# Optimization experiments

Measured on AMD Instinct MI355X. Metric: run time of the kernel, lower is better.

Reference implementation:

```python
import jax, jax.numpy as jnp
import numpy as np

D_MODEL = 2048
D_HEAD = 64
Q_HEADS = 32
KV_HEADS = 8


def rope(x):
    # x: [B, S, H, D], rotate interleaved pairs along last dim
    B, S, H, D = x.shape
    pos = jnp.arange(S, dtype=x.dtype)
    freq = 1.0 / (10000.0 ** (jnp.arange(0, D, 2, dtype=x.dtype) / D))  # [D/2]
    theta = pos[:, None] * freq[None, :]                                 # [S, D/2]
    cos = jnp.cos(theta)[None, :, None, :]
    sin = jnp.sin(theta)[None, :, None, :]
    xr = x.reshape(B, S, H, D // 2, 2)
    x1, x2 = xr[..., 0], xr[..., 1]
    out = jnp.stack((x1 * cos - x2 * sin, x1 * sin + x2 * cos), axis=-1)
    return out.reshape(B, S, H, D)


def setup_inputs() -> dict:
    key = jax.random.key(0)
    ks = jax.random.split(key, 7)
    x = jax.random.normal(ks[0], (1, 2048, D_MODEL), dtype=jnp.float32)
    W_q = jax.random.normal(ks[1], (Q_HEADS * D_HEAD, D_MODEL), dtype=jnp.float32) * 0.02
    b_q = jnp.zeros((Q_HEADS * D_HEAD,), dtype=jnp.float32)
    W_kv = jax.random.normal(ks[2], (2 * KV_HEADS * D_HEAD, D_MODEL), dtype=jnp.float32) * 0.02
    b_kv = jnp.zeros((2 * KV_HEADS * D_HEAD,), dtype=jnp.float32)
    W_out = jax.random.normal(ks[3], (D_MODEL, D_MODEL), dtype=jnp.float32) * 0.02
    b_out = jnp.zeros((D_MODEL,), dtype=jnp.float32)
    return {"x": x, "W_q": W_q, "b_q": b_q, "W_kv": W_kv, "b_kv": b_kv,
            "W_out": W_out, "b_out": b_out}


def reference(x, W_q, b_q, W_kv, b_kv, W_out, b_out):
    B, S, _ = x.shape
    g = Q_HEADS // KV_HEADS
    Q = (x @ W_q.T + b_q).reshape(B, S, Q_HEADS, D_HEAD)
    kv = x @ W_kv.T + b_kv
    K, V = jnp.split(kv, 2, axis=-1)
    K = K.reshape(B, S, KV_HEADS, D_HEAD)
    V = V.reshape(B, S, KV_HEADS, D_HEAD)
    Q = rope(Q)
    K = rope(K)
    K = jnp.repeat(K, g, axis=2)  # [B, S, Q_HEADS, D_HEAD]
    V = jnp.repeat(V, g, axis=2)
    scale = 1.0 / (D_HEAD ** 0.5)
    scores = jnp.einsum('bqhd,bkhd->bhqk', Q, K) * scale  # [B,H,S,S]
    # note: original calls non-inplace masked_fill and discards it, so no causal mask applied
    probs = jax.nn.softmax(scores, axis=-1)
    attn = jnp.einsum('bhqk,bkhd->bqhd', probs, V).reshape(B, S, D_MODEL)
    return attn @ W_out.T + b_out
```

## Files before the change

### kernel.cpp

```cpp
#include <hip/hip_runtime.h>
#include <hip/hip_bf16.h>
#include <math.h>

#define S_LEN 2048
#define D_MODEL 2048
#define Q_HEADS 32
#define KV_HEADS 8

typedef __attribute__((ext_vector_type(8))) short short8;
typedef __attribute__((ext_vector_type(4))) float f32x4;

__device__ __forceinline__ short bf16_rne(float f) {
  unsigned u = __float_as_uint(f);
  unsigned r = (u + 0x7FFFu + ((u >> 16) & 1u)) >> 16;
  return (short)r;
}
__device__ __forceinline__ void dma16(const short* g, short* l) {
  __builtin_amdgcn_global_load_lds(
      (const __attribute__((address_space(1))) void*)g,
      (__attribute__((address_space(3))) void*)l, 16, 0, 0);
}
__device__ __forceinline__ void fast_sincos(float theta, float& sn, float& cs) {
  double rev = (double)theta * 0.15915494309189535;
  float fr = (float)(rev - floor(rev));
  sn = __builtin_amdgcn_sinf(fr);
  cs = __builtin_amdgcn_cosf(fr);
}
__device__ __forceinline__ void cvt8(const float* src, short* dst, int i) {
  float4 a = *(const float4*)&src[i];
  float4 b = *(const float4*)&src[i + 4];
  short8 h;
  h[0] = bf16_rne(a.x); h[1] = bf16_rne(a.y);
  h[2] = bf16_rne(a.z); h[3] = bf16_rne(a.w);
  h[4] = bf16_rne(b.x); h[5] = bf16_rne(b.y);
  h[6] = bf16_rne(b.z); h[7] = bf16_rne(b.w);
  *(short8*)&dst[i] = h;
}

#define NM (2048 * 2048)
#define NKV (1024 * 2048)

__global__ __launch_bounds__(256) void cvt_all(
    const float* __restrict__ x,    short* __restrict__ xh,
    const float* __restrict__ wq,   short* __restrict__ wqh,
    const float* __restrict__ wkv,  short* __restrict__ wkvh,
    const float* __restrict__ wo,   short* __restrict__ woh,
    float* __restrict__ freqTab) {
  if (blockIdx.x == 0 && threadIdx.x < 32) {
    const double e = (2.0 * threadIdx.x) / 64.0;
    freqTab[threadIdx.x] = (float)pow(10000.0, -e);
  }
  int i = (blockIdx.x * 256 + threadIdx.x) * 8;
  if (i < NM) { cvt8(x, xh, i); return; }
  i -= NM;
  if (i < NM) { cvt8(wq, wqh, i); return; }
  i -= NM;
  if (i < NKV) { cvt8(wkv, wkvh, i); return; }
  i -= NKV;
  cvt8(wo, woh, i);
}

#define QSCALE 0.18033688011112042f

__global__ __launch_bounds__(256) void gemm_qkv_rope(
    const short* __restrict__ Ah,
    const short* __restrict__ Bq, const short* __restrict__ Bkv,
    const float* __restrict__ bq, const float* __restrict__ bkv,
    const float* __restrict__ tab,
    short* __restrict__ Qrm, short* __restrict__ Krm,
    short* __restrict__ Vt) {
  const int Nq = 2048, K = 2048;
  __shared__ short As[2][128 * 32];
  __shared__ short Bs[2][64 * 32];
  const int tid = threadIdx.x;
  const int w = tid >> 6, lane = tid & 63;
  const int l16 = lane & 15, quad = lane >> 4;

  const int b = blockIdx.x;
  const int r = b & 7, ri = b >> 3;
  const int bx = (r & 3) * 12 + ri % 12;
  const int by = (r >> 2) * 8 + ri / 12;
  const int bm = by * 128;
  const int bnG = bx * 64;

  const short* Bsrc; const float* bias; int bn;
  if (bnG < Nq) { Bsrc = Bq;  bias = bq;  bn = bnG; }
  else          { Bsrc = Bkv; bias = bkv; bn = bnG - Nq; }
  const int mode = (bnG < Nq) ? 0 : ((bnG < Nq + 512) ? 1 : 2);

  const int drow0 = w * 16 + (lane >> 2);
  const int drow1 = drow0 + 64;
  const int slot = lane & 3;
  const int ch0 = slot ^ ((drow0 >> 1) & 3);
  const int ch1 = slot ^ ((drow1 >> 1) & 3);
  const size_t a0 = (size_t)(bm + drow0) * K + ch0 * 8;
  const size_t a1 = (size_t)(bm + drow1) * K + ch1 * 8;
  const size_t b0 = (size_t)(bn + drow0) * K + ch0 * 8;
  const int dA0 = (w * 16) * 32, dA1 = (64 + w * 16) * 32;

  const int wm = (w & 1) * 64, wn = (w >> 1) * 32;
  int offA[4], offB[2];
#pragma unroll
  for (int i = 0; i < 4; ++i) {
    int R = wm + i * 16 + l16;
    offA[i] = R * 32 + (quad ^ ((R >> 1) & 3)) * 8;
  }
#pragma unroll
  for (int j = 0; j < 2; ++j) {
    int R = wn + j * 16 + l16;
    offB[j] = R * 32 + (quad ^ ((R >> 1) & 3)) * 8;
  }

  f32x4 acc[4][2];
#pragma unroll
  for (int i = 0; i < 4; ++i)
#pragma unroll
    for (int j = 0; j < 2; ++j)
#pragma unroll
      for (int e = 0; e < 4; ++e) acc[i][j][e] = 0.f;

  const int T = K / 32;
  dma16(Ah + a0, &As[0][dA0]);
  dma16(Ah + a1, &As[0][dA1]);
  dma16(Bsrc + b0, &Bs[0][dA0]);
  __syncthreads();

  for (int t = 0; t < T; ++t) {
    const int cur = t & 1, nxt = cur ^ 1;
    if (t + 1 < T) {
      const int ko = (t + 1) * 32;
      dma16(Ah + a0 + ko, &As[nxt][dA0]);
      dma16(Ah + a1 + ko, &As[nxt][dA1]);
      dma16(Bsrc + b0 + ko, &Bs[nxt][dA0]);
    }
    short8 af[4], bf[2];
#pragma unroll
    for (int i = 0; i < 4; ++i) af[i] = *(const short8*)&As[cur][offA[i]];
#pragma unroll
    for (int j = 0; j < 2; ++j) bf[j] = *(const short8*)&Bs[cur][offB[j]];
#pragma unroll
    for (int i = 0; i < 4; ++i)
#pragma unroll
      for (int j = 0; j < 2; ++j)
        acc[i][j] = __builtin_amdgcn_mfma_f32_16x16x32_bf16(af[i], bf[j], acc[i][j], 0, 0, 0);
    __syncthreads();
  }

#pragma unroll
  for (int i = 0; i < 4; ++i) {
    const int row0 = bm + wm + i * 16 + quad * 4;
#pragma unroll
    for (int j = 0; j < 2; ++j) {
      const int col = bn + wn + j * 16 + l16;
      const float bv = bias[col];
      if (mode == 2) {
        const int d = col - 512;
        short4 sv;
        sv.x = bf16_rne(acc[i][j][0] + bv);
        sv.y = bf16_rne(acc[i][j][1] + bv);
        sv.z = bf16_rne(acc[i][j][2] + bv);
        sv.w = bf16_rne(acc[i][j][3] + bv);
        *(short4*)&Vt[(size_t)d * S_LEN + row0] = sv;
      } else {
        const float fr = tab[(col & 63) >> 1];
        const float sgn = (col & 1) ? 1.f : -1.f;
#pragma unroll
        for (int e = 0; e < 4; ++e) {
          float v = acc[i][j][e] + bv;
          float other = __shfl_xor(v, 1);
          float sn, cs;
          fast_sincos((float)(row0 + e) * fr, sn, cs);
          const float o = v * cs + sgn * other * sn;
          if (mode == 0)
            Qrm[(size_t)(row0 + e) * D_MODEL + col] = bf16_rne(o * QSCALE);
          else
            Krm[(size_t)(row0 + e) * 512 + col] = bf16_rne(o);
        }
      }
    }
  }
}

__global__ __launch_bounds__(256) void gemm_nt1_big(
    const short* __restrict__ A, const short* __restrict__ B,
    const float* __restrict__ bias, float* __restrict__ C,
    int N, int K) {
  __shared__ short As[2][128 * 32];
  __shared__ short Bs[2][128 * 32];
  const int tid = threadIdx.x;
  const int w = tid >> 6, lane = tid & 63;
  const int l16 = lane & 15, quad = lane >> 4;

  const int b = blockIdx.x;
  const int r = b & 7, ri = b >> 3;
  const int bx = (r & 1) * 8 + ri % 8;
  const int by = (r >> 1) * 4 + ri / 8;
  const int bm = by * 128;
  const int bn = bx * 128;

  const int drow0 = w * 16 + (lane >> 2);
  const int drow1 = drow0 + 64;
  const int slot = lane & 3;
  const int ch0 = slot ^ ((drow0 >> 1) & 3);
  const int ch1 = slot ^ ((drow1 >> 1) & 3);
  const short* gA0 = &A[(size_t)(bm + drow0) * K + ch0 * 8];
  const short* gA1 = &A[(size_t)(bm + drow1) * K + ch1 * 8];
  const short* gB0 = &B[(size_t)(bn + drow0) * K + ch0 * 8];
  const short* gB1 = &B[(size_t)(bn + drow1) * K + ch1 * 8];
  const int dA0 = (w * 16) * 32, dA1 = (64 + w * 16) * 32;

  const int wm = (w & 1) * 64, wn = (w >> 1) * 64;
  int offA[4], offB[4];
#pragma unroll
  for (int i = 0; i < 4; ++i) {
    int R = wm + i * 16 + l16;
    offA[i] = R * 32 + (quad ^ ((R >> 1) & 3)) * 8;
    int Rb = wn + i * 16 + l16;
    offB[i] = Rb * 32 + (quad ^ ((Rb >> 1) & 3)) * 8;
  }

  f32x4 acc[4][4];
#pragma unroll
  for (int i = 0; i < 4; ++i)
#pragma unroll
    for (int j = 0; j < 4; ++j)
#pragma unroll
      for (int e = 0; e < 4; ++e) acc[i][j][e] = 0.f;

  const int T = K / 32;
  dma16(gA0, &As[0][dA0]);
  dma16(gA1, &As[0][dA1]);
  dma16(gB0, &Bs[0][dA0]);
  dma16(gB1, &Bs[0][dA1]);
  __syncthreads();

  for (int t = 0; t < T; ++t) {
    const int cur = t & 1, nxt = cur ^ 1;
    if (t + 1 < T) {
      const int ko = (t + 1) * 32;
      dma16(gA0 + ko, &As[nxt][dA0]);
      dma16(gA1 + ko, &As[nxt][dA1]);
      dma16(gB0 + ko, &Bs[nxt][dA0]);
      dma16(gB1 + ko, &Bs[nxt][dA1]);
    }
    short8 af[4], bf[4];
#pragma unroll
    for (int i = 0; i < 4; ++i) af[i] = *(const short8*)&As[cur][offA[i]];
#pragma unroll
    for (int j = 0; j < 4; ++j) bf[j] = *(const short8*)&Bs[cur][offB[j]];
#pragma unroll
    for (int i = 0; i < 4; ++i)
#pragma unroll
      for (int j = 0; j < 4; ++j)
        acc[i][j] = __builtin_amdgcn_mfma_f32_16x16x32_bf16(af[i], bf[j], acc[i][j], 0, 0, 0);
    __syncthreads();
  }

#pragma unroll
  for (int i = 0; i < 4; ++i) {
#pragma unroll
    for (int j = 0; j < 4; ++j) {
      const int col = bn + wn + j * 16 + l16;
      const float bv = bias[col];
      const int row0 = bm + wm + i * 16 + quad * 4;
#pragma unroll
      for (int e = 0; e < 4; ++e)
        C[(size_t)(row0 + e) * N + col] = acc[i][j][e] + bv;
    }
  }
}

__global__ __launch_bounds__(256, 4) void flash8(
    const short* __restrict__ Qrm, const short* __restrict__ Krm,
    const short* __restrict__ Vt, short* __restrict__ Oh) {
  const int qt = blockIdx.x, h = blockIdx.y;
  const int kvh = h >> 2;
  const int tid = threadIdx.x;
  const int w = tid >> 6, lane = tid & 63;
  const int l16 = lane & 15, quad = lane >> 4;

  __shared__ short Ks[2][64 * 64];
  __shared__ short Vs[2][64 * 64];
  __shared__ short Ps[64 * 64];

  const short* Vh = Vt + (size_t)kvh * 64 * S_LEN;
  const int qr = qt * 64 + w * 16 + l16;

  short8 qf0 = *(const short8*)&Qrm[(size_t)qr * D_MODEL + h * 64 + quad * 8];
  short8 qf1 = *(const short8*)&Qrm[(size_t)qr * D_MODEL + h * 64 + 32 + quad * 8];

  short8 ones;
#pragma unroll
  for (int e = 0; e < 8; ++e) ones[e] = (short)0x3F80;

  const int drow = lane >> 3;
  const int ch = (lane & 7) ^ drow;
  const short* gK = &Krm[(size_t)(w * 16 + drow) * 512 + kvh * 64 + ch * 8];
  const short* gV = &Vh[(size_t)(w * 16 + drow) * S_LEN + ch * 8];

  const int sl0 = quad ^ (l16 & 7);
  int offT[4][2];
#pragma unroll
  for (int m = 0; m < 4; ++m) {
    offT[m][0] = (m * 16 + l16) * 64 + sl0 * 8;
    offT[m][1] = (m * 16 + l16) * 64 + (sl0 ^ 4) * 8;
  }

  const int prow = (w * 16 + l16) * 64;
  const int pswz = (l16 & 7) << 1;
  int pwr[4];
#pragma unroll
  for (int m = 0; m < 4; ++m) pwr[m] = prow + ((4 * m + quad) ^ pswz) * 4;
  const int prd0 = prow + ((2 * quad) ^ pswz) * 4;
  const int prd1 = prow + ((8 + 2 * quad) ^ pswz) * 4;

  f32x4 accl;
#pragma unroll
  for (int e = 0; e < 4; ++e) accl[e] = 0.f;
  f32x4 acco[4];
#pragma unroll
  for (int m = 0; m < 4; ++m)
#pragma unroll
    for (int e = 0; e < 4; ++e) acco[m][e] = 0.f;

  dma16(gK,               &Ks[0][(w * 16) * 64]);
  dma16(gK + 8 * 512,     &Ks[0][(w * 16 + 8) * 64]);
  dma16(gV,               &Vs[0][(w * 16) * 64]);
  dma16(gV + 8 * S_LEN,   &Vs[0][(w * 16 + 8) * 64]);
  __syncthreads();

  for (int t = 0; t < 32; ++t) {
    const int cur = t & 1, nxt = cur ^ 1;
    if (t + 1 < 32) {
      const short* gKn = gK + (size_t)(t + 1) * 64 * 512;
      const short* gVn = gV + (t + 1) * 64;
      dma16(gKn,             &Ks[nxt][(w * 16) * 64]);
      dma16(gKn + 8 * 512,   &Ks[nxt][(w * 16 + 8) * 64]);
      dma16(gVn,             &Vs[nxt][(w * 16) * 64]);
      dma16(gVn + 8 * S_LEN, &Vs[nxt][(w * 16 + 8) * 64]);
    }

    const short* kc = Ks[cur];
    f32x4 accs[4];
#pragma unroll
    for (int m = 0; m < 4; ++m)
#pragma unroll
      for (int e = 0; e < 4; ++e) accs[m][e] = 0.f;
#pragma unroll
    for (int m = 0; m < 4; ++m) {
      short8 k0 = *(const short8*)&kc[offT[m][0]];
      short8 k1 = *(const short8*)&kc[offT[m][1]];
      accs[m] = __builtin_amdgcn_mfma_f32_16x16x32_bf16(k0, qf0, accs[m], 0, 0, 0);
      accs[m] = __builtin_amdgcn_mfma_f32_16x16x32_bf16(k1, qf1, accs[m], 0, 0, 0);
    }

#pragma unroll
    for (int m = 0; m < 4; ++m) {
      float p0 = exp2f(accs[m][0]);
      float p1 = exp2f(accs[m][1]);
      float p2 = exp2f(accs[m][2]);
      float p3 = exp2f(accs[m][3]);
      unsigned u01 = __builtin_amdgcn_perm(__float_as_uint(p1), __float_as_uint(p0), 0x07060302u);
      unsigned u23 = __builtin_amdgcn_perm(__float_as_uint(p3), __float_as_uint(p2), 0x07060302u);
      *(uint2*)&Ps[pwr[m]] = make_uint2(u01, u23);
    }

    short8 pf0 = *(const short8*)&Ps[prd0];
    short8 pf1 = *(const short8*)&Ps[prd1];
    accl = __builtin_amdgcn_mfma_f32_16x16x32_bf16(ones, pf0, accl, 0, 0, 0);
    accl = __builtin_amdgcn_mfma_f32_16x16x32_bf16(ones, pf1, accl, 0, 0, 0);
    const short* vc = Vs[cur];
#pragma unroll
    for (int m = 0; m < 4; ++m) {
      short8 v0 = *(const short8*)&vc[offT[m][0]];
      short8 v1 = *(const short8*)&vc[offT[m][1]];
      acco[m] = __builtin_amdgcn_mfma_f32_16x16x32_bf16(v0, pf0, acco[m], 0, 0, 0);
      acco[m] = __builtin_amdgcn_mfma_f32_16x16x32_bf16(v1, pf1, acco[m], 0, 0, 0);
    }

    __syncthreads();
  }

  const float inv = 1.f / accl[0];
#pragma unroll
  for (int m = 0; m < 4; ++m) {
    short4 h4;
    h4.x = bf16_rne(acco[m][0] * inv);
    h4.y = bf16_rne(acco[m][1] * inv);
    h4.z = bf16_rne(acco[m][2] * inv);
    h4.w = bf16_rne(acco[m][3] * inv);
    const size_t base = (size_t)qr * D_MODEL + h * 64 + m * 16 + quad * 4;
    *(short4*)&Oh[base] = h4;
  }
}

extern "C" void kernel_launch(void* const* d_in, const int* in_sizes, int n_in,
                              void* d_out, int out_size, void* d_ws, size_t ws_size,
                              hipStream_t stream) {
  const float* x     = (const float*)d_in[0];
  const float* W_q   = (const float*)d_in[1];
  const float* b_q   = (const float*)d_in[2];
  const float* W_kv  = (const float*)d_in[3];
  const float* b_kv  = (const float*)d_in[4];
  const float* W_out = (const float*)d_in[5];
  const float* b_out = (const float*)d_in[6];
  float* out = (float*)d_out;

  char* ws = (char*)d_ws;
  short* xh    = (short*)(ws);
  short* Wqh   = (short*)(ws + (8u << 20));
  short* Wkvh  = (short*)(ws + (16u << 20));
  short* Woh   = (short*)(ws + (20u << 20));
  short* Qrm   = (short*)(ws + (28u << 20));
  short* Krm   = (short*)(ws + (36u << 20));
  short* Vtb   = (short*)(ws + (38u << 20));
  float* freqTab = (float*)(ws + (40u << 20));
  short* Ath   = xh;

  cvt_all<<<7168, 256, 0, stream>>>(x, xh, W_q, Wqh, W_kv, Wkvh, W_out, Woh,
                                    freqTab);

  gemm_qkv_rope<<<768, 256, 0, stream>>>(
      xh, Wqh, Wkvh, b_q, b_kv, freqTab, Qrm, Krm, Vtb);

  flash8<<<dim3(S_LEN / 64, Q_HEADS), 256, 0, stream>>>(Qrm, Krm, Vtb, Ath);

  gemm_nt1_big<<<256, 256, 0, stream>>>(Ath, Woh, b_out, out, 2048, 2048);
}
```

Measured before the change: 256.3 us.

## Double flash attention KV tile to 128 keys per iteration

The attention kernel now processes 128 keys per loop iteration instead of 64, halving the number of iterations and barriers. K, V and P shared buffers double in size, with new swizzled offsets and DMA addressing for the wider V tile. Score accumulation is fused per 16-key block so exp2 and P stores follow each MFMA pair directly. LDS use doubles and launch bounds drop to 2 blocks per CU, which may reduce occupancy and latency hiding.

```diff
diff --git a/kernel.cpp b/kernel.cpp
--- a/kernel.cpp
+++ b/kernel.cpp
@@ -270,7 +270,7 @@
   }
 }
 
-__global__ __launch_bounds__(256, 4) void flash8(
+__global__ __launch_bounds__(256, 2) void flash9(
     const short* __restrict__ Qrm, const short* __restrict__ Krm,
     const short* __restrict__ Vt, short* __restrict__ Oh) {
   const int qt = blockIdx.x, h = blockIdx.y;
@@ -279,9 +279,9 @@
   const int w = tid >> 6, lane = tid & 63;
   const int l16 = lane & 15, quad = lane >> 4;
 
-  __shared__ short Ks[2][64 * 64];
-  __shared__ short Vs[2][64 * 64];
-  __shared__ short Ps[64 * 64];
+  __shared__ short Ks[2][128 * 64];
+  __shared__ short Vs[2][64 * 128];
+  __shared__ short Ps[64 * 128];
 
   const short* Vh = Vt + (size_t)kvh * 64 * S_LEN;
   const int qr = qt * 64 + w * 16 + l16;
@@ -293,26 +293,42 @@
 #pragma unroll
   for (int e = 0; e < 8; ++e) ones[e] = (short)0x3F80;
 
-  const int drow = lane >> 3;
-  const int ch = (lane & 7) ^ drow;
-  const short* gK = &Krm[(size_t)(w * 16 + drow) * 512 + kvh * 64 + ch * 8];
-  const short* gV = &Vh[(size_t)(w * 16 + drow) * S_LEN + ch * 8];
+  f32x4 fz;
+#pragma unroll
+  for (int e = 0; e < 4; ++e) fz[e] = 0.f;
+
+  const int drK = lane >> 3;
+  const short* gK = &Krm[(size_t)(w * 32 + drK) * 512 + kvh * 64 +
+                         ((lane & 7) ^ drK) * 8];
+  const int drV = lane >> 4;
+  const short* gVa = &Vh[(size_t)(w * 16 + drV) * S_LEN +
+                         (((lane & 15) ^ drV)) * 8];
+  const short* gVb = &Vh[(size_t)(w * 16 + drV) * S_LEN +
+                         (((lane & 15) ^ drV ^ 4)) * 8];
 
   const int sl0 = quad ^ (l16 & 7);
-  int offT[4][2];
-#pragma unroll
-  for (int m = 0; m < 4; ++m) {
-    offT[m][0] = (m * 16 + l16) * 64 + sl0 * 8;
-    offT[m][1] = (m * 16 + l16) * 64 + (sl0 ^ 4) * 8;
-  }
-
-  const int prow = (w * 16 + l16) * 64;
+  int offK[8][2];
+#pragma unroll
+  for (int m = 0; m < 8; ++m) {
+    offK[m][0] = (m * 16 + l16) * 64 + sl0 * 8;
+    offK[m][1] = (m * 16 + l16) * 64 + (sl0 ^ 4) * 8;
+  }
+  int offV[4][4];
+#pragma unroll
+  for (int m = 0; m < 4; ++m)
+#pragma unroll
+    for (int ks = 0; ks < 4; ++ks)
+      offV[m][ks] = (m * 16 + l16) * 128 + ((4 * ks + quad) ^ (l16 & 7)) * 8;
+
+  const int prow = (w * 16 + l16) * 128;
   const int pswz = (l16 & 7) << 1;
-  int pwr[4];
-#pragma unroll
-  for (int m = 0; m < 4; ++m) pwr[m] = prow + ((4 * m + quad) ^ pswz) * 4;
-  const int prd0 = prow + ((2 * quad) ^ pswz) * 4;
-  const int prd1 = prow + ((8 + 2 * quad) ^ pswz) * 4;
+  int pwr[8];
+#pragma unroll
+  for (int m = 0; m < 8; ++m) pwr[m] = prow + ((4 * m + quad) ^ pswz) * 4;
+  int prd[4];
+#pragma unroll
+  for (int ks = 0; ks < 4; ++ks)
+    prd[ks] = prow + ((8 * ks + 2 * quad) ^ pswz) * 4;
 
   f32x4 accl;
 #pragma unroll
@@ -323,59 +339,61 @@
 #pragma unroll
     for (int e = 0; e < 4; ++e) acco[m][e] = 0.f;
 
-  dma16(gK,               &Ks[0][(w * 16) * 64]);
-  dma16(gK + 8 * 512,     &Ks[0][(w * 16 + 8) * 64]);
-  dma16(gV,               &Vs[0][(w * 16) * 64]);
-  dma16(gV + 8 * S_LEN,   &Vs[0][(w * 16 + 8) * 64]);
+#pragma unroll
+  for (int d8 = 0; d8 < 4; ++d8)
+    dma16(gK + d8 * 8 * 512, &Ks[0][(w * 32 + d8 * 8) * 64]);
+  dma16(gVa,                &Vs[0][(w * 16 + 0) * 128]);
+  dma16(gVb + 4 * S_LEN,    &Vs[0][(w * 16 + 4) * 128]);
+  dma16(gVa + 8 * S_LEN,    &Vs[0][(w * 16 + 8) * 128]);
+  dma16(gVb + 12 * S_LEN,   &Vs[0][(w * 16 + 12) * 128]);
   __syncthreads();
 
-  for (int t = 0; t < 32; ++t) {
+  for (int t = 0; t < 16; ++t) {
     const int cur = t & 1, nxt = cur ^ 1;
-    if (t + 1 < 32) {
-      const short* gKn = gK + (size_t)(t + 1) * 64 * 512;
-      const short* gVn = gV + (t + 1) * 64;
-      dma16(gKn,             &Ks[nxt][(w * 16) * 64]);
-      dma16(gKn + 8 * 512,   &Ks[nxt][(w * 16 + 8) * 64]);
-      dma16(gVn,             &Vs[nxt][(w * 16) * 64]);
-      dma16(gVn + 8 * S_LEN, &Vs[nxt][(w * 16 + 8) * 64]);
+    if (t + 1 < 16) {
+      const short* gKn = gK + (size_t)(t + 1) * 128 * 512;
+      const short* gVna = gVa + (t + 1) * 128;
+      const short* gVnb = gVb + (t + 1) * 128;
+#pragma unroll
+      for (int d8 = 0; d8 < 4; ++d8)
+        dma16(gKn + d8 * 8 * 512, &Ks[nxt][(w * 32 + d8 * 8) * 64]);
+      dma16(gVna,              &Vs[nxt][(w * 16 + 0) * 128]);
+      dma16(gVnb + 4 * S_LEN,  &Vs[nxt][(w * 16 + 4) * 128]);
+      dma16(gVna + 8 * S_LEN,  &Vs[nxt][(w * 16 + 8) * 128]);
+      dma16(gVnb + 12 * S_LEN, &Vs[nxt][(w * 16 + 12) * 128]);
     }
 
     const short* kc = Ks[cur];
-    f32x4 accs[4];
-#pragma unroll
-    for (int m = 0; m < 4; ++m)
-#pragma unroll
-      for (int e = 0; e < 4; ++e) accs[m][e] = 0.f;
-#pragma unroll
-    for (int m = 0; m < 4; ++m) {
-      short8 k0 = *(const short8*)&kc[offT[m][0]];
-      short8 k1 = *(const short8*)&kc[offT[m][1]];
-      accs[m] = __builtin_amdgcn_mfma_f32_16x16x32_bf16(k0, qf0, accs[m], 0, 0, 0);
-      accs[m] = __builtin_amdgcn_mfma_f32_16x16x32_bf16(k1, qf1, accs[m], 0, 0, 0);
-    }
-
-#pragma unroll
-    for (int m = 0; m < 4; ++m) {
-      float p0 = exp2f(accs[m][0]);
-      float p1 = exp2f(accs[m][1]);
-      float p2 = exp2f(accs[m][2]);
-      float p3 = exp2f(accs[m][3]);
+#pragma unroll
+    for (int m = 0; m < 8; ++m) {
+      short8 k0 = *(const short8*)&kc[offK[m][0]];
+      short8 k1 = *(const short8*)&kc[offK[m][1]];
+      f32x4 s = __builtin_amdgcn_mfma_f32_16x16x32_bf16(k0, qf0, fz, 0, 0, 0);
+      s = __builtin_amdgcn_mfma_f32_16x16x32_bf16(k1, qf1, s, 0, 0, 0);
+      float p0 = exp2f(s[0]);
+      float p1 = exp2f(s[1]);
+      float p2 = exp2f(s[2]);
+      float p3 = exp2f(s[3]);
       unsigned u01 = __builtin_amdgcn_perm(__float_as_uint(p1), __float_as_uint(p0), 0x07060302u);
       unsigned u23 = __builtin_amdgcn_perm(__float_as_uint(p3), __float_as_uint(p2), 0x07060302u);
       *(uint2*)&Ps[pwr[m]] = make_uint2(u01, u23);
     }
 
-    short8 pf0 = *(const short8*)&Ps[prd0];
-    short8 pf1 = *(const short8*)&Ps[prd1];
-    accl = __builtin_amdgcn_mfma_f32_16x16x32_bf16(ones, pf0, accl, 0, 0, 0);
-    accl = __builtin_amdgcn_mfma_f32_16x16x32_bf16(ones, pf1, accl, 0, 0, 0);
+    short8 pf[4];
+#pragma unroll
+    for (int ks = 0; ks < 4; ++ks) pf[ks] = *(const short8*)&Ps[prd[ks]];
+#pragma unroll
+    for (int ks = 0; ks < 4; ++ks)
+      accl = __builtin_amdgcn_mfma_f32_16x16x32_bf16(ones, pf[ks], accl, 0, 0, 0);
+
     const short* vc = Vs[cur];
 #pragma unroll
     for (int m = 0; m < 4; ++m) {
-      short8 v0 = *(const short8*)&vc[offT[m][0]];
-      short8 v1 = *(const short8*)&vc[offT[m][1]];
-      acco[m] = __builtin_amdgcn_mfma_f32_16x16x32_bf16(v0, pf0, acco[m], 0, 0, 0);
-      acco[m] = __builtin_amdgcn_mfma_f32_16x16x32_bf16(v1, pf1, acco[m], 0, 0, 0);
+#pragma unroll
+      for (int ks = 0; ks < 4; ++ks) {
+        short8 vf = *(const short8*)&vc[offV[m][ks]];
+        acco[m] = __builtin_amdgcn_mfma_f32_16x16x32_bf16(vf, pf[ks], acco[m], 0, 0, 0);
+      }
     }
 
     __syncthreads();
@@ -423,7 +441,7 @@
   gemm_qkv_rope<<<768, 256, 0, stream>>>(
       xh, Wqh, Wkvh, b_q, b_kv, freqTab, Qrm, Krm, Vtb);
 
-  flash8<<<dim3(S_LEN / 64, Q_HEADS), 256, 0, stream>>>(Qrm, Krm, Vtb, Ath);
+  flash9<<<dim3(S_LEN / 64, Q_HEADS), 256, 0, stream>>>(Qrm, Krm, Vtb, Ath);
 
   gemm_nt1_big<<<256, 256, 0, stream>>>(Ath, Woh, b_out, out, 2048, 2048);
 }
```

After: 262.6 us. 1.02x slower.
